# Optimization experiments

Hardware: AMD Instinct MI355X
Metric: run time of the kernel (lower is better)

Reference implementation:

```python
import jax, jax.numpy as jnp
import numpy as np

N, H, W = 128, 64, 64
CH_I, CH_H, CH_Q = 2, 150, 10
N_ACT = 8


def conv3x3(x, w):
    # x: [N,H,W,Cin], w: [3,3,Cin,Cout], 'same' padding, stride 1
    return jax.lax.conv_general_dilated(
        x, w, window_strides=(1, 1), padding='SAME',
        dimension_numbers=('NHWC', 'HWIO', 'NHWC'))


def setup_inputs() -> dict:
    key = jax.random.key(0)
    ks = jax.random.split(key, 9)
    std = 0.01
    x = jax.random.normal(ks[0], (N, H, W, CH_I), dtype=jnp.float32)
    S1 = jax.random.randint(ks[1], (N,), 0, H, dtype=jnp.int32)
    S2 = jax.random.randint(ks[2], (N,), 0, W, dtype=jnp.int32)
    w0 = std * jax.random.normal(ks[3], (3, 3, CH_I, CH_H), dtype=jnp.float32)
    b0 = jnp.zeros((CH_H,), dtype=jnp.float32)
    w_r = std * jax.random.normal(ks[4], (3, 3, CH_H, 1), dtype=jnp.float32)
    w_q = std * jax.random.normal(ks[5], (3, 3, 2, CH_Q), dtype=jnp.float32)
    w_sw = std * jax.random.normal(ks[6], (3, 3, 2, CH_Q), dtype=jnp.float32)
    w_sw2 = std * jax.random.normal(ks[7], (3, 3, 2, CH_Q), dtype=jnp.float32)
    w_dense = std * jax.random.normal(ks[8], (CH_Q, N_ACT), dtype=jnp.float32)
    return {"x": x, "S1": S1, "S2": S2, "VInum": 36,
            "w0": w0, "b0": b0, "w_r": w_r, "w_q": w_q,
            "w_sw": w_sw, "w_sw2": w_sw2, "w_dense": w_dense}


def reference(x, S1, S2, VInum, w0, b0, w_r, w_q, w_sw, w_sw2, w_dense):
    k = int(VInum)
    h = conv3x3(x, w0) + b0                      # [N,H,W,ch_h]
    r = conv3x3(h, w_r)                          # [N,H,W,1] reward map
    v = jnp.zeros_like(r)
    # first VI step uses conv2 weights
    q = conv3x3(jnp.concatenate([r, v], axis=3), w_q)
    v = jnp.max(q, axis=3, keepdims=True)
    # k-1 shared-weight value-iteration steps
    def body(v, _):
        q = conv3x3(jnp.concatenate([r, v], axis=3), w_sw)
        return jnp.max(q, axis=3, keepdims=True), None
    v, _ = jax.lax.scan(body, v, None, length=k - 1)
    # final step with second shared-weight conv
    q = conv3x3(jnp.concatenate([r, v], axis=3), w_sw2)  # [N,H,W,ch_q]
    # attention: gather Q values at state (S1,S2) per batch element
    q_out = q[jnp.arange(q.shape[0]), S1, S2]            # [N,ch_q]
    logits = q_out @ w_dense                             # [N,8]
    prob_actions = jax.nn.softmax(logits, axis=-1)
    return (logits, prob_actions, q, q_out)
```

## Files before the change

kernel.cpp:

```cpp
#include <hip/hip_runtime.h>
#include <math.h>


#define XROW 69
#define VROW 67
#define VSTR (66 * VROW)

__global__ void
__attribute__((amdgpu_flat_work_group_size(512, 512)))
__attribute__((amdgpu_waves_per_eu(2, 2)))
vin_kernel(const float* __restrict__ x,
           const int* __restrict__ S1,
           const int* __restrict__ S2,
           const int* __restrict__ VInum,
           const float* __restrict__ w0,
           const float* __restrict__ b0,
           const float* __restrict__ w_r,
           const float* __restrict__ w_q,
           const float* __restrict__ w_sw,
           const float* __restrict__ w_sw2,
           const float* __restrict__ w_dense,
           float* __restrict__ out) {
    const int b = blockIdx.x;
    const int t = threadIdx.x;

    __shared__ float xs0[68 * XROW];
    __shared__ float xs1[68 * XROW];
    __shared__ float rs[66 * VROW];
    __shared__ float vpool[2 * VSTR];
    __shared__ float wtA[1620];
    __shared__ float Pp[450];
    __shared__ float Bt[90];
    __shared__ float Bv[9];
    __shared__ float W5c[459];
    __shared__ float swv[90];
    __shared__ float qsel[10];

    for (int i = t; i < 68 * XROW; i += 512) { xs0[i] = 0.f; xs1[i] = 0.f; }
    for (int i = t; i < 66 * VROW; i += 512) rs[i] = 0.f;
    for (int i = t; i < 2 * VSTR; i += 512) vpool[i] = 0.f;
    if (t < 450) Pp[t] = 0.f;
    if (t < 90) swv[t] = w_sw[(t / 10) * 20 + 10 + (t % 10)];
    __syncthreads();

    const int row = t >> 3;
    const int cb  = (t & 7) << 3;

    {
        const float* xb = x + (size_t)b * 64 * 64 * 2;
        const float4* xp = (const float4*)(xb + (row * 64 + cb) * 2);
        #pragma unroll
        for (int g = 0; g < 4; ++g) {
            float4 v4 = xp[g];
            int px = cb + g * 2;
            xs0[(row + 2) * XROW + px + 2] = v4.x;
            xs1[(row + 2) * XROW + px + 2] = v4.y;
            xs0[(row + 2) * XROW + px + 3] = v4.z;
            xs1[(row + 2) * XROW + px + 3] = v4.w;
        }
    }
    for (int idx = t; idx < 1620; idx += 512) {
        int entry = idx / 10, ch = idx - entry * 10;
        int d = entry / 18, rem = entry % 18;
        int uu = rem >> 1, ci = rem & 1;
        int c0 = ch * 15;
        const float* wr = w_r + d * 150;
        const float* wp = w0 + (uu * 2 + ci) * 150;
        float s = 0.f;
        for (int c = c0; c < c0 + 15; ++c) s += wr[c] * wp[c];
        wtA[idx] = s;
    }
    if (t < 90) {
        int d = t / 10, ch = t - d * 10, c0 = ch * 15;
        float s = 0.f;
        for (int c = c0; c < c0 + 15; ++c) s += w_r[d * 150 + c] * b0[c];
        Bt[t] = s;
    }
    __syncthreads();
    if (t < 162) {
        float s = 0.f;
        #pragma unroll
        for (int i = 0; i < 10; ++i) s += wtA[t * 10 + i];
        int d = t / 18, rem = t % 18;
        int uu = rem >> 1, ci = rem & 1;
        int dy = d / 3 - 1, dx = d % 3 - 1;
        int uy = uu / 3 - 1, ux = uu % 3 - 1;
        int eidx = (dy + uy + 2) * 5 + (dx + ux + 2);
        Pp[d * 50 + eidx * 2 + ci] = s;
    } else if (t >= 256 && t < 265) {
        int d = t - 256;
        float s = 0.f;
        #pragma unroll
        for (int i = 0; i < 10; ++i) s += Bt[d * 10 + i];
        Bv[d] = s;
    }
    __syncthreads();
    if (t < 459) {
        int cls = t / 51, j = t - cls * 51;
        int cy = cls / 3, cx = cls % 3;
        float s = 0.f;
        #pragma unroll
        for (int d = 0; d < 9; ++d) {
            int dy = d / 3 - 1, dx = d % 3 - 1;
            bool ok = (cy == 0 || (cy == 1 ? dy >= 0 : dy <= 0)) &&
                      (cx == 0 || (cx == 1 ? dx >= 0 : dx <= 0));
            if (ok) s += (j < 50) ? Pp[d * 50 + j] : Bv[d];
        }
        W5c[t] = s;
    }
    __syncthreads();

    {
        int cy = (row == 0) ? 1 : (row == 63) ? 2 : 0;
        #pragma unroll
        for (int p = 0; p < 8; ++p) {
            int xx = cb + p;
            int cx = (xx == 0) ? 1 : (xx == 63) ? 2 : 0;
            const float* Wp = &W5c[(cy * 3 + cx) * 51];
            float acc = Wp[50];
            #pragma unroll
            for (int e = 0; e < 25; ++e) {
                int xi = (row + e / 5) * XROW + (xx + e % 5);
                acc = fmaf(xs0[xi], Wp[e * 2], acc);
                acc = fmaf(xs1[xi], Wp[e * 2 + 1], acc);
            }
            rs[(row + 1) * VROW + (xx + 1)] = acc;
        }
    }
    __syncthreads();

    const int K = VInum[0];

    float Rsw[8][10];
    {
        float rwin[3][10];
        #pragma unroll
        for (int i = 0; i < 3; ++i) {
            const float* rp = &rs[(row + i) * VROW + cb];
            #pragma unroll
            for (int j = 0; j < 10; ++j) rwin[i][j] = rp[j];
        }
        float vmax[8];
        #pragma unroll
        for (int a = 0; a < 10; ++a) {
            #pragma unroll
            for (int p = 0; p < 8; ++p) {
                float accR = 0.f, accQ = 0.f;
                #pragma unroll
                for (int d = 0; d < 9; ++d) {
                    float rv = rwin[d / 3][p + d % 3];
                    accR = fmaf(w_sw[d * 20 + a], rv, accR);
                    accQ = fmaf(w_q[d * 20 + a],  rv, accQ);
                }
                Rsw[p][a] = accR;
                vmax[p] = (a == 0) ? accQ : fmaxf(vmax[p], accQ);
            }
        }
        #pragma unroll
        for (int p = 0; p < 8; ++p)
            vpool[0 * VSTR + (row + 1) * VROW + (cb + p + 1)] = vmax[p];
    }
    __syncthreads();

    int cur = 0;
    for (int it = 0; it < K - 1; ++it) {
        const float* vb = &vpool[cur * VSTR + row * VROW + cb];
        float vwin[3][10];
        #pragma unroll
        for (int i = 0; i < 3; ++i)
            #pragma unroll
            for (int j = 0; j < 10; ++j) vwin[i][j] = vb[i * VROW + j];
        int nxt = cur ^ 1;
        float vmax[8];
        #pragma unroll
        for (int a = 0; a < 10; ++a) {
            #pragma unroll
            for (int p = 0; p < 8; ++p) {
                float acc = Rsw[p][a];
                #pragma unroll
                for (int d = 0; d < 9; ++d)
                    acc = fmaf(swv[d * 10 + a], vwin[d / 3][p + d % 3], acc);
                vmax[p] = (a == 0) ? acc : fmaxf(vmax[p], acc);
            }
        }
        #pragma unroll
        for (int p = 0; p < 8; ++p)
            vpool[nxt * VSTR + (row + 1) * VROW + (cb + p + 1)] = vmax[p];
        cur = nxt;
        __syncthreads();
    }

    const int s1 = S1[b], s2 = S2[b];
    {
        float rwin[3][10], vwin[3][10];
        #pragma unroll
        for (int i = 0; i < 3; ++i) {
            const float* rp = &rs[(row + i) * VROW + cb];
            const float* vb = &vpool[cur * VSTR + (row + i) * VROW + cb];
            #pragma unroll
            for (int j = 0; j < 10; ++j) { rwin[i][j] = rp[j]; vwin[i][j] = vb[j]; }
        }
        float qv[8][10];
        #pragma unroll
        for (int a = 0; a < 10; ++a) {
            #pragma unroll
            for (int p = 0; p < 8; ++p) {
                float acc = 0.f;
                #pragma unroll
                for (int d = 0; d < 9; ++d) {
                    acc = fmaf(w_sw2[d * 20 + a],      rwin[d / 3][p + d % 3], acc);
                    acc = fmaf(w_sw2[d * 20 + 10 + a], vwin[d / 3][p + d % 3], acc);
                }
                qv[p][a] = acc;
            }
        }
        {
            float4* qp4 = (float4*)(out + 2048 + ((size_t)((b * 64 + row) * 64 + cb)) * 10);
            #pragma unroll
            for (int g = 0; g < 20; ++g)
                qp4[g] = make_float4(qv[(g * 4) / 10][(g * 4) % 10],
                                     qv[(g * 4 + 1) / 10][(g * 4 + 1) % 10],
                                     qv[(g * 4 + 2) / 10][(g * 4 + 2) % 10],
                                     qv[(g * 4 + 3) / 10][(g * 4 + 3) % 10]);
        }
        if (row == s1) {
            #pragma unroll
            for (int p = 0; p < 8; ++p)
                if (s2 == cb + p) {
                    #pragma unroll
                    for (int a = 0; a < 10; ++a) qsel[a] = qv[p][a];
                }
        }
    }
    __syncthreads();

    if (t == 0) {
        float logits[8];
        float m = -1e30f;
        #pragma unroll
        for (int j = 0; j < 8; ++j) {
            float s = 0.f;
            #pragma unroll
            for (int a = 0; a < 10; ++a) s += qsel[a] * w_dense[a * 8 + j];
            logits[j] = s;
            m = fmaxf(m, s);
        }
        float sum = 0.f;
        float e[8];
        #pragma unroll
        for (int j = 0; j < 8; ++j) { e[j] = expf(logits[j] - m); sum += e[j]; }
        float inv = 1.f / sum;
        #pragma unroll
        for (int j = 0; j < 8; ++j) {
            out[b * 8 + j] = logits[j];
            out[1024 + b * 8 + j] = e[j] * inv;
        }
    }
    if (t < 10) out[5244928 + b * 10 + t] = qsel[t];
}

extern "C" void kernel_launch(void* const* d_in, const int* in_sizes, int n_in,
                              void* d_out, int out_size, void* d_ws, size_t ws_size,
                              hipStream_t stream) {
    const float* x      = (const float*)d_in[0];
    const int*   S1     = (const int*)d_in[1];
    const int*   S2     = (const int*)d_in[2];
    const int*   VInum  = (const int*)d_in[3];
    const float* w0     = (const float*)d_in[4];
    const float* b0     = (const float*)d_in[5];
    const float* w_r    = (const float*)d_in[6];
    const float* w_q    = (const float*)d_in[7];
    const float* w_sw   = (const float*)d_in[8];
    const float* w_sw2  = (const float*)d_in[9];
    const float* w_dense= (const float*)d_in[10];
    float* out = (float*)d_out;

    vin_kernel<<<128, 512, 0, stream>>>(x, S1, S2, VInum, w0, b0, w_r, w_q,
                                        w_sw, w_sw2, w_dense, out);
}
```

Baseline: 200.1 us.

## Split each batch image across two workgroups with periodic halo exchange

Launches 256 cooperative workgroups, two per batch image, so twice as many compute units share the value-iteration loop. Each workgroup updates its own half of the rows plus a shrinking 8-row halo. Every 8 iterations the two partners swap boundary rows through global workspace memory, using release/acquire flags and spin-waiting. The cost is redundant halo compute, a fully duplicated prologue, an extra flag-init launch and cross-workgroup synchronisation. It falls back to the original single-workgroup kernel when the workspace is too small.

```diff
diff --git a/kernel.cpp b/kernel.cpp
--- a/kernel.cpp
+++ b/kernel.cpp
@@ -5,24 +5,121 @@
 #define XROW 69
 #define VROW 67
 #define VSTR (66 * VROW)
+#define PAY_FLOATS (256 * 2 * 512)
+#define WS_NEED_BYTES ((PAY_FLOATS + 256) * 4)
+
+__global__ void init_flags(int* flags) { flags[threadIdx.x] = 0; }
+
+#define VIN_PROLOGUE(NTHR)                                                    \
+    for (int i = t; i < 68 * XROW; i += NTHR) { xs0[i] = 0.f; xs1[i] = 0.f; } \
+    for (int i = t; i < 66 * VROW; i += NTHR) rs[i] = 0.f;                    \
+    for (int i = t; i < 2 * VSTR; i += NTHR) vpool[i] = 0.f;                  \
+    if (t < 450) Pp[t] = 0.f;                                                 \
+    if (t < 90) swv[t] = w_sw[(t / 10) * 20 + 10 + (t % 10)];                 \
+    __syncthreads();                                                          \
+    {                                                                         \
+        const float* xb = x + (size_t)b * 64 * 64 * 2;                        \
+        const float4* xp = (const float4*)(xb + (rowP * 64 + cbP) * 2);       \
+        _Pragma("unroll")                                                     \
+        for (int g = 0; g < 4; ++g) {                                         \
+            float4 v4 = xp[g];                                                \
+            int px = cbP + g * 2;                                             \
+            xs0[(rowP + 2) * XROW + px + 2] = v4.x;                           \
+            xs1[(rowP + 2) * XROW + px + 2] = v4.y;                           \
+            xs0[(rowP + 2) * XROW + px + 3] = v4.z;                           \
+            xs1[(rowP + 2) * XROW + px + 3] = v4.w;                           \
+        }                                                                     \
+    }                                                                         \
+    for (int w = t; w < 1620; w += NTHR) {                                    \
+        int entry = w / 10, ch = w - entry * 10;                              \
+        int d = entry / 18, rem = entry % 18;                                 \
+        int uu = rem >> 1, ci = rem & 1;                                      \
+        int c0 = ch * 15;                                                     \
+        const float* wr = w_r + d * 150;                                      \
+        const float* wp = w0 + (uu * 2 + ci) * 150;                           \
+        float s = 0.f;                                                        \
+        for (int c = c0; c < c0 + 15; ++c) s += wr[c] * wp[c];                \
+        wtA[w] = s;                                                           \
+    }                                                                         \
+    if (t < 90) {                                                             \
+        int d = t / 10, ch = t - d * 10, c0 = ch * 15;                        \
+        float s = 0.f;                                                        \
+        for (int c = c0; c < c0 + 15; ++c) s += w_r[d * 150 + c] * b0[c];     \
+        Bt[t] = s;                                                            \
+    }                                                                         \
+    __syncthreads();                                                          \
+    if (t < 162) {                                                            \
+        float s = 0.f;                                                        \
+        _Pragma("unroll")                                                     \
+        for (int i = 0; i < 10; ++i) s += wtA[t * 10 + i];                    \
+        int d = t / 18, rem = t % 18;                                         \
+        int uu = rem >> 1, ci = rem & 1;                                      \
+        int dy = d / 3 - 1, dx = d % 3 - 1;                                   \
+        int uy = uu / 3 - 1, ux = uu % 3 - 1;                                 \
+        int eidx = (dy + uy + 2) * 5 + (dx + ux + 2);                         \
+        Pp[d * 50 + eidx * 2 + ci] = s;                                       \
+    } else if (t >= 256 && t < 265) {                                         \
+        int d = t - 256;                                                      \
+        float s = 0.f;                                                        \
+        _Pragma("unroll")                                                     \
+        for (int i = 0; i < 10; ++i) s += Bt[d * 10 + i];                     \
+        Bv[d] = s;                                                            \
+    }                                                                         \
+    __syncthreads();                                                          \
+    if (t < 459) {                                                            \
+        int cls = t / 51, j = t - cls * 51;                                   \
+        int cy = cls / 3, cx = cls % 3;                                       \
+        float s = 0.f;                                                        \
+        _Pragma("unroll")                                                     \
+        for (int d = 0; d < 9; ++d) {                                         \
+            int dy = d / 3 - 1, dx = d % 3 - 1;                               \
+            bool ok = (cy == 0 || (cy == 1 ? dy >= 0 : dy <= 0)) &&           \
+                      (cx == 0 || (cx == 1 ? dx >= 0 : dx <= 0));             \
+            if (ok) s += (j < 50) ? Pp[d * 50 + j] : Bv[d];                   \
+        }                                                                     \
+        W5c[t] = s;                                                           \
+    }                                                                         \
+    __syncthreads();                                                          \
+    {                                                                         \
+        int cy = (rowP == 0) ? 1 : (rowP == 63) ? 2 : 0;                      \
+        _Pragma("unroll")                                                     \
+        for (int p = 0; p < 8; ++p) {                                         \
+            int xx = cbP + p;                                                 \
+            int cx = (xx == 0) ? 1 : (xx == 63) ? 2 : 0;                      \
+            const float* Wp = &W5c[(cy * 3 + cx) * 51];                       \
+            float acc = Wp[50];                                               \
+            _Pragma("unroll")                                                 \
+            for (int e = 0; e < 25; ++e) {                                    \
+                int xi = (rowP + e / 5) * XROW + (xx + e % 5);                \
+                acc = fmaf(xs0[xi], Wp[e * 2], acc);                          \
+                acc = fmaf(xs1[xi], Wp[e * 2 + 1], acc);                      \
+            }                                                                 \
+            rs[(rowP + 1) * VROW + (xx + 1)] = acc;                           \
+        }                                                                     \
+    }                                                                         \
+    __syncthreads();
 
 __global__ void
 __attribute__((amdgpu_flat_work_group_size(512, 512)))
 __attribute__((amdgpu_waves_per_eu(2, 2)))
-vin_kernel(const float* __restrict__ x,
-           const int* __restrict__ S1,
-           const int* __restrict__ S2,
-           const int* __restrict__ VInum,
-           const float* __restrict__ w0,
-           const float* __restrict__ b0,
-           const float* __restrict__ w_r,
-           const float* __restrict__ w_q,
-           const float* __restrict__ w_sw,
-           const float* __restrict__ w_sw2,
-           const float* __restrict__ w_dense,
-           float* __restrict__ out) {
-    const int b = blockIdx.x;
+vin_split(const float* __restrict__ x,
+          const int* __restrict__ S1,
+          const int* __restrict__ S2,
+          const int* __restrict__ VInum,
+          const float* __restrict__ w0,
+          const float* __restrict__ b0,
+          const float* __restrict__ w_r,
+          const float* __restrict__ w_q,
+          const float* __restrict__ w_sw,
+          const float* __restrict__ w_sw2,
+          const float* __restrict__ w_dense,
+          float* __restrict__ wsf,
+          float* __restrict__ out) {
+    const int wg = blockIdx.x;
+    const int b = wg >> 1, h = wg & 1;
+    const int partner = wg ^ 1;
     const int t = threadIdx.x;
+    int* flags = (int*)(wsf + PAY_FLOATS);
 
     __shared__ float xs0[68 * XROW];
     __shared__ float xs1[68 * XROW];
@@ -36,100 +133,14 @@
     __shared__ float swv[90];
     __shared__ float qsel[10];
 
-    for (int i = t; i < 68 * XROW; i += 512) { xs0[i] = 0.f; xs1[i] = 0.f; }
-    for (int i = t; i < 66 * VROW; i += 512) rs[i] = 0.f;
-    for (int i = t; i < 2 * VSTR; i += 512) vpool[i] = 0.f;
-    if (t < 450) Pp[t] = 0.f;
-    if (t < 90) swv[t] = w_sw[(t / 10) * 20 + 10 + (t % 10)];
-    __syncthreads();
-
+    const int rowP = t >> 3;
+    const int cbP  = (t & 7) << 3;
+
+    VIN_PROLOGUE(512)
+
+    const int K = VInum[0];
     const int row = t >> 3;
     const int cb  = (t & 7) << 3;
-
-    {
-        const float* xb = x + (size_t)b * 64 * 64 * 2;
-        const float4* xp = (const float4*)(xb + (row * 64 + cb) * 2);
-        #pragma unroll
-        for (int g = 0; g < 4; ++g) {
-            float4 v4 = xp[g];
-            int px = cb + g * 2;
-            xs0[(row + 2) * XROW + px + 2] = v4.x;
-            xs1[(row + 2) * XROW + px + 2] = v4.y;
-            xs0[(row + 2) * XROW + px + 3] = v4.z;
-            xs1[(row + 2) * XROW + px + 3] = v4.w;
-        }
-    }
-    for (int idx = t; idx < 1620; idx += 512) {
-        int entry = idx / 10, ch = idx - entry * 10;
-        int d = entry / 18, rem = entry % 18;
-        int uu = rem >> 1, ci = rem & 1;
-        int c0 = ch * 15;
-        const float* wr = w_r + d * 150;
-        const float* wp = w0 + (uu * 2 + ci) * 150;
-        float s = 0.f;
-        for (int c = c0; c < c0 + 15; ++c) s += wr[c] * wp[c];
-        wtA[idx] = s;
-    }
-    if (t < 90) {
-        int d = t / 10, ch = t - d * 10, c0 = ch * 15;
-        float s = 0.f;
-        for (int c = c0; c < c0 + 15; ++c) s += w_r[d * 150 + c] * b0[c];
-        Bt[t] = s;
-    }
-    __syncthreads();
-    if (t < 162) {
-        float s = 0.f;
-        #pragma unroll
-        for (int i = 0; i < 10; ++i) s += wtA[t * 10 + i];
-        int d = t / 18, rem = t % 18;
-        int uu = rem >> 1, ci = rem & 1;
-        int dy = d / 3 - 1, dx = d % 3 - 1;
-        int uy = uu / 3 - 1, ux = uu % 3 - 1;
-        int eidx = (dy + uy + 2) * 5 + (dx + ux + 2);
-        Pp[d * 50 + eidx * 2 + ci] = s;
-    } else if (t >= 256 && t < 265) {
-        int d = t - 256;
-        float s = 0.f;
-        #pragma unroll
-        for (int i = 0; i < 10; ++i) s += Bt[d * 10 + i];
-        Bv[d] = s;
-    }
-    __syncthreads();
-    if (t < 459) {
-        int cls = t / 51, j = t - cls * 51;
-        int cy = cls / 3, cx = cls % 3;
-        float s = 0.f;
-        #pragma unroll
-        for (int d = 0; d < 9; ++d) {
-            int dy = d / 3 - 1, dx = d % 3 - 1;
-            bool ok = (cy == 0 || (cy == 1 ? dy >= 0 : dy <= 0)) &&
-                      (cx == 0 || (cx == 1 ? dx >= 0 : dx <= 0));
-            if (ok) s += (j < 50) ? Pp[d * 50 + j] : Bv[d];
-        }
-        W5c[t] = s;
-    }
-    __syncthreads();
-
-    {
-        int cy = (row == 0) ? 1 : (row == 63) ? 2 : 0;
-        #pragma unroll
-        for (int p = 0; p < 8; ++p) {
-            int xx = cb + p;
-            int cx = (xx == 0) ? 1 : (xx == 63) ? 2 : 0;
-            const float* Wp = &W5c[(cy * 3 + cx) * 51];
-            float acc = Wp[50];
-            #pragma unroll
-            for (int e = 0; e < 25; ++e) {
-                int xi = (row + e / 5) * XROW + (xx + e % 5);
-                acc = fmaf(xs0[xi], Wp[e * 2], acc);
-                acc = fmaf(xs1[xi], Wp[e * 2 + 1], acc);
-            }
-            rs[(row + 1) * VROW + (xx + 1)] = acc;
-        }
-    }
-    __syncthreads();
-
-    const int K = VInum[0];
 
     float Rsw[8][10];
     {
@@ -162,6 +173,213 @@
     }
     __syncthreads();
 
+    int cur = 0, m = 8, chunk = 0;
+    for (int it = 0; it < K - 1; ++it) {
+        int nxt = cur ^ 1;
+        bool active = h ? (row >= 33 - m) : (row < 31 + m);
+        if (active) {
+            const float* vb = &vpool[cur * VSTR + row * VROW + cb];
+            float vwin[3][10];
+            #pragma unroll
+            for (int i = 0; i < 3; ++i)
+                #pragma unroll
+                for (int j = 0; j < 10; ++j) vwin[i][j] = vb[i * VROW + j];
+            float vmax[8];
+            #pragma unroll
+            for (int a = 0; a < 10; ++a) {
+                #pragma unroll
+                for (int p = 0; p < 8; ++p) {
+                    float acc = Rsw[p][a];
+                    #pragma unroll
+                    for (int d = 0; d < 9; ++d)
+                        acc = fmaf(swv[d * 10 + a], vwin[d / 3][p + d % 3], acc);
+                    vmax[p] = (a == 0) ? acc : fmaxf(vmax[p], acc);
+                }
+            }
+            #pragma unroll
+            for (int p = 0; p < 8; ++p)
+                vpool[nxt * VSTR + (row + 1) * VROW + (cb + p + 1)] = vmax[p];
+        }
+        cur = nxt;
+        m -= 1;
+        __syncthreads();
+
+        if (m == 0) {
+            ++chunk;
+            int par = chunk & 1;
+            if (t < 128) {
+                int lr2 = t >> 4, col = (t & 15) << 2;
+                int srow = (h ? 32 : 24) + lr2;
+                const float* sp = &vpool[cur * VSTR + (srow + 1) * VROW + col + 1];
+                float* dp = wsf + ((size_t)(wg * 2 + par)) * 512 + t * 4;
+                dp[0] = sp[0]; dp[1] = sp[1]; dp[2] = sp[2]; dp[3] = sp[3];
+            }
+            __syncthreads();
+            if (t == 0) {
+                __threadfence();
+                __hip_atomic_store(&flags[wg], chunk, __ATOMIC_RELEASE,
+                                   __HIP_MEMORY_SCOPE_AGENT);
+                while (__hip_atomic_load(&flags[partner], __ATOMIC_RELAXED,
+                                         __HIP_MEMORY_SCOPE_AGENT) < chunk)
+                    __builtin_amdgcn_s_sleep(2);
+                (void)__hip_atomic_load(&flags[partner], __ATOMIC_ACQUIRE,
+                                        __HIP_MEMORY_SCOPE_AGENT);
+            }
+            __syncthreads();
+            if (t < 128) {
+                int lr2 = t >> 4, col = (t & 15) << 2;
+                int rrow = (h ? 24 : 32) + lr2;
+                const float* sp = wsf + ((size_t)(partner * 2 + par)) * 512 + t * 4;
+                float v0 = __hip_atomic_load(&sp[0], __ATOMIC_RELAXED, __HIP_MEMORY_SCOPE_AGENT);
+                float v1 = __hip_atomic_load(&sp[1], __ATOMIC_RELAXED, __HIP_MEMORY_SCOPE_AGENT);
+                float v2 = __hip_atomic_load(&sp[2], __ATOMIC_RELAXED, __HIP_MEMORY_SCOPE_AGENT);
+                float v3 = __hip_atomic_load(&sp[3], __ATOMIC_RELAXED, __HIP_MEMORY_SCOPE_AGENT);
+                float* dp = &vpool[cur * VSTR + (rrow + 1) * VROW + col + 1];
+                dp[0] = v0; dp[1] = v1; dp[2] = v2; dp[3] = v3;
+            }
+            m = 8;
+            __syncthreads();
+        }
+    }
+
+    const int s1 = S1[b], s2 = S2[b];
+    const bool owner = ((s1 >> 5) == h);
+    if ((row >> 5) == h) {
+        float rwin[3][10], vwin[3][10];
+        #pragma unroll
+        for (int i = 0; i < 3; ++i) {
+            const float* rp = &rs[(row + i) * VROW + cb];
+            const float* vb = &vpool[cur * VSTR + (row + i) * VROW + cb];
+            #pragma unroll
+            for (int j = 0; j < 10; ++j) { rwin[i][j] = rp[j]; vwin[i][j] = vb[j]; }
+        }
+        float qv[8][10];
+        #pragma unroll
+        for (int a = 0; a < 10; ++a) {
+            #pragma unroll
+            for (int p = 0; p < 8; ++p) {
+                float acc = 0.f;
+                #pragma unroll
+                for (int d = 0; d < 9; ++d) {
+                    acc = fmaf(w_sw2[d * 20 + a],      rwin[d / 3][p + d % 3], acc);
+                    acc = fmaf(w_sw2[d * 20 + 10 + a], vwin[d / 3][p + d % 3], acc);
+                }
+                qv[p][a] = acc;
+            }
+        }
+        float4* qp4 = (float4*)(out + 2048 + ((size_t)((b * 64 + row) * 64 + cb)) * 10);
+        #pragma unroll
+        for (int g = 0; g < 20; ++g)
+            qp4[g] = make_float4(qv[(g * 4) / 10][(g * 4) % 10],
+                                 qv[(g * 4 + 1) / 10][(g * 4 + 1) % 10],
+                                 qv[(g * 4 + 2) / 10][(g * 4 + 2) % 10],
+                                 qv[(g * 4 + 3) / 10][(g * 4 + 3) % 10]);
+        if (owner && row == s1) {
+            #pragma unroll
+            for (int p = 0; p < 8; ++p)
+                if (s2 == cb + p) {
+                    #pragma unroll
+                    for (int a = 0; a < 10; ++a) qsel[a] = qv[p][a];
+                }
+        }
+    }
+    __syncthreads();
+
+    if (owner && t == 0) {
+        float logits[8];
+        float mx = -1e30f;
+        #pragma unroll
+        for (int j = 0; j < 8; ++j) {
+            float s = 0.f;
+            #pragma unroll
+            for (int a = 0; a < 10; ++a) s += qsel[a] * w_dense[a * 8 + j];
+            logits[j] = s;
+            mx = fmaxf(mx, s);
+        }
+        float sum = 0.f;
+        float e[8];
+        #pragma unroll
+        for (int j = 0; j < 8; ++j) { e[j] = expf(logits[j] - mx); sum += e[j]; }
+        float inv = 1.f / sum;
+        #pragma unroll
+        for (int j = 0; j < 8; ++j) {
+            out[b * 8 + j] = logits[j];
+            out[1024 + b * 8 + j] = e[j] * inv;
+        }
+    }
+    if (owner && t < 10) out[5244928 + b * 10 + t] = qsel[t];
+}
+
+__global__ void
+__attribute__((amdgpu_flat_work_group_size(512, 512)))
+__attribute__((amdgpu_waves_per_eu(2, 2)))
+vin_full(const float* __restrict__ x,
+         const int* __restrict__ S1,
+         const int* __restrict__ S2,
+         const int* __restrict__ VInum,
+         const float* __restrict__ w0,
+         const float* __restrict__ b0,
+         const float* __restrict__ w_r,
+         const float* __restrict__ w_q,
+         const float* __restrict__ w_sw,
+         const float* __restrict__ w_sw2,
+         const float* __restrict__ w_dense,
+         float* __restrict__ out) {
+    const int b = blockIdx.x;
+    const int t = threadIdx.x;
+
+    __shared__ float xs0[68 * XROW];
+    __shared__ float xs1[68 * XROW];
+    __shared__ float rs[66 * VROW];
+    __shared__ float vpool[2 * VSTR];
+    __shared__ float wtA[1620];
+    __shared__ float Pp[450];
+    __shared__ float Bt[90];
+    __shared__ float Bv[9];
+    __shared__ float W5c[459];
+    __shared__ float swv[90];
+    __shared__ float qsel[10];
+
+    const int rowP = t >> 3;
+    const int cbP  = (t & 7) << 3;
+
+    VIN_PROLOGUE(512)
+
+    const int K = VInum[0];
+    const int row = t >> 3;
+    const int cb  = (t & 7) << 3;
+
+    float Rsw[8][10];
+    {
+        float rwin[3][10];
+        #pragma unroll
+        for (int i = 0; i < 3; ++i) {
+            const float* rp = &rs[(row + i) * VROW + cb];
+            #pragma unroll
+            for (int j = 0; j < 10; ++j) rwin[i][j] = rp[j];
+        }
+        float vmax[8];
+        #pragma unroll
+        for (int a = 0; a < 10; ++a) {
+            #pragma unroll
+            for (int p = 0; p < 8; ++p) {
+                float accR = 0.f, accQ = 0.f;
+                #pragma unroll
+                for (int d = 0; d < 9; ++d) {
+                    float rv = rwin[d / 3][p + d % 3];
+                    accR = fmaf(w_sw[d * 20 + a], rv, accR);
+                    accQ = fmaf(w_q[d * 20 + a],  rv, accQ);
+                }
+                Rsw[p][a] = accR;
+                vmax[p] = (a == 0) ? accQ : fmaxf(vmax[p], accQ);
+            }
+        }
+        #pragma unroll
+        for (int p = 0; p < 8; ++p)
+            vpool[0 * VSTR + (row + 1) * VROW + (cb + p + 1)] = vmax[p];
+    }
+    __syncthreads();
+
     int cur = 0;
     for (int it = 0; it < K - 1; ++it) {
         const float* vb = &vpool[cur * VSTR + row * VROW + cb];
@@ -214,15 +432,13 @@
                 qv[p][a] = acc;
             }
         }
-        {
-            float4* qp4 = (float4*)(out + 2048 + ((size_t)((b * 64 + row) * 64 + cb)) * 10);
-            #pragma unroll
-            for (int g = 0; g < 20; ++g)
-                qp4[g] = make_float4(qv[(g * 4) / 10][(g * 4) % 10],
-                                     qv[(g * 4 + 1) / 10][(g * 4 + 1) % 10],
-                                     qv[(g * 4 + 2) / 10][(g * 4 + 2) % 10],
-                                     qv[(g * 4 + 3) / 10][(g * 4 + 3) % 10]);
-        }
+        float4* qp4 = (float4*)(out + 2048 + ((size_t)((b * 64 + row) * 64 + cb)) * 10);
+        #pragma unroll
+        for (int g = 0; g < 20; ++g)
+            qp4[g] = make_float4(qv[(g * 4) / 10][(g * 4) % 10],
+                                 qv[(g * 4 + 1) / 10][(g * 4 + 1) % 10],
+                                 qv[(g * 4 + 2) / 10][(g * 4 + 2) % 10],
+                                 qv[(g * 4 + 3) / 10][(g * 4 + 3) % 10]);
         if (row == s1) {
             #pragma unroll
             for (int p = 0; p < 8; ++p)
@@ -236,19 +452,19 @@
 
     if (t == 0) {
         float logits[8];
-        float m = -1e30f;
+        float mx = -1e30f;
         #pragma unroll
         for (int j = 0; j < 8; ++j) {
             float s = 0.f;
             #pragma unroll
             for (int a = 0; a < 10; ++a) s += qsel[a] * w_dense[a * 8 + j];
             logits[j] = s;
-            m = fmaxf(m, s);
+            mx = fmaxf(mx, s);
         }
         float sum = 0.f;
         float e[8];
         #pragma unroll
-        for (int j = 0; j < 8; ++j) { e[j] = expf(logits[j] - m); sum += e[j]; }
+        for (int j = 0; j < 8; ++j) { e[j] = expf(logits[j] - mx); sum += e[j]; }
         float inv = 1.f / sum;
         #pragma unroll
         for (int j = 0; j < 8; ++j) {
@@ -274,7 +490,18 @@
     const float* w_sw2  = (const float*)d_in[9];
     const float* w_dense= (const float*)d_in[10];
     float* out = (float*)d_out;
-
-    vin_kernel<<<128, 512, 0, stream>>>(x, S1, S2, VInum, w0, b0, w_r, w_q,
-                                        w_sw, w_sw2, w_dense, out);
+    float* wsf = (float*)d_ws;
+
+    if (ws_size >= (size_t)WS_NEED_BYTES) {
+        init_flags<<<1, 256, 0, stream>>>((int*)(wsf + PAY_FLOATS));
+        void* args[] = {(void*)&x, (void*)&S1, (void*)&S2, (void*)&VInum,
+                        (void*)&w0, (void*)&b0, (void*)&w_r, (void*)&w_q,
+                        (void*)&w_sw, (void*)&w_sw2, (void*)&w_dense,
+                        (void*)&wsf, (void*)&out};
+        hipLaunchCooperativeKernel((const void*)vin_split, dim3(256), dim3(512),
+                                   args, 0, stream);
+    } else {
+        vin_full<<<128, 512, 0, stream>>>(x, S1, S2, VInum, w0, b0, w_r, w_q,
+                                          w_sw, w_sw2, w_dense, out);
+    }
 }
```

New measurement: 273.8 us. 1.37x slower.
